# Optimization experiments

Measured on AMD Instinct MI355X. Metric: run time of the kernel, lower is better.

## Reference

```python
import jax, jax.numpy as jnp
import numpy as np

HEADS = 8
DIM_HEAD = 64
NB_FEATURES = 256
DIM = 512

def setup_inputs() -> dict:
    key = jax.random.key(0)
    ks = jax.random.split(key, 4)
    b, n = 2, 8192
    x = jax.random.normal(ks[0], (b, n, DIM), jnp.float32)
    # fan-in scaling so exp(feature projections) stays numerically sane
    Wqkv = jax.random.normal(ks[1], (3 * HEADS * DIM_HEAD, DIM), jnp.float32) / np.sqrt(DIM).astype(np.float32)
    Wout = jax.random.normal(ks[2], (DIM, HEADS * DIM_HEAD), jnp.float32) / np.sqrt(HEADS * DIM_HEAD).astype(np.float32)
    bout = jnp.zeros((DIM,), jnp.float32)
    proj = jax.random.normal(ks[3], (NB_FEATURES, DIM_HEAD), jnp.float32) / np.sqrt(DIM_HEAD).astype(np.float32)
    return {"x": x, "Wqkv": Wqkv, "Wout": Wout, "bout": bout, "proj": proj}

def reference(x, Wqkv, Wout, bout, proj):
    b, n, _ = x.shape
    scale = DIM_HEAD ** -0.5
    qkv = jnp.einsum('bnd,ed->bne', x, Wqkv)            # [b,n,3*h*dh]
    q, k, v = jnp.split(qkv, 3, axis=-1)
    to_heads = lambda t: t.reshape(b, n, HEADS, DIM_HEAD).transpose(0, 2, 1, 3)  # [b,h,n,dh]
    q = to_heads(q) * scale
    k = to_heads(k)
    v = to_heads(v)
    # FAVOR+ exp feature maps
    q_prime = jnp.exp(jnp.einsum('bhnd,fd->bhnf', q, proj))  # [b,h,n,f]
    k_prime = jnp.exp(jnp.einsum('bhnd,fd->bhnf', k, proj))  # [b,h,n,f]
    k_sum = k_prime.sum(axis=2)                              # [b,h,f]
    D = jnp.einsum('bhnf,bhf->bhn', q_prime, k_sum)          # normalizer
    D_inv = 1.0 / (D + 1e-6)
    context = jnp.einsum('bhmf,bhmd->bhfd', k_prime, v)      # [b,h,f,dh]
    out = jnp.einsum('bhnf,bhfd->bhnd', q_prime, context) * D_inv[..., None]
    out = out.transpose(0, 2, 1, 3).reshape(b, n, HEADS * DIM_HEAD)
    return jnp.einsum('bne,de->bnd', out, Wout) + bout
```

## Files before the change

kernel.cpp:

```cpp
#include <hip/hip_runtime.h>
#include <math.h>

#define B_    2
#define NSEQ  8192
#define DIM_  512
#define H_    8
#define DH_   64
#define F_    256
#define M_    (B_*NSEQ)
#define QKV_  1536

typedef __attribute__((ext_vector_type(8))) short     short8;
typedef __attribute__((ext_vector_type(4))) float     float4v;
typedef __attribute__((ext_vector_type(8))) unsigned short ushort8v;

__device__ __forceinline__ unsigned short f2bf(float f) {
    unsigned u = __float_as_uint(f);
    u += 0x7FFFu + ((u >> 16) & 1u);
    return (unsigned short)(u >> 16);
}
__device__ __forceinline__ float bf2f(unsigned short h) {
    unsigned u = ((unsigned)h) << 16;
    return __uint_as_float(u);
}
__device__ __forceinline__ unsigned pack2bf(float lo, float hi) {
    return __builtin_amdgcn_perm(__float_as_uint(hi), __float_as_uint(lo), 0x07060302);
}
__device__ __forceinline__ void glds16(const void* g, void* s) {
    __builtin_amdgcn_global_load_lds(
        (const __attribute__((address_space(1))) unsigned int*)g,
        (__attribute__((address_space(3))) unsigned int*)s, 16, 0, 0);
}

__global__ __launch_bounds__(256) void cvt_all(const float* __restrict__ x,
                                               const float* __restrict__ wqkv,
                                               const float* __restrict__ wout,
                                               const float* __restrict__ proj,
                                               unsigned short* __restrict__ xb,
                                               unsigned short* __restrict__ wqkvb,
                                               unsigned short* __restrict__ woutb,
                                               unsigned short* __restrict__ projb) {
    int bid = blockIdx.x;
    const float* in; unsigned short* out; int i;
    if (bid < 4096)      { in = x;    out = xb;    i = bid * 256 + threadIdx.x; }
    else if (bid < 4480) { in = wqkv; out = wqkvb; i = (bid - 4096) * 256 + threadIdx.x; }
    else if (bid < 4608) { in = wout; out = woutb; i = (bid - 4480) * 256 + threadIdx.x; }
    else                 { in = proj; out = projb; i = (bid - 4608) * 256 + threadIdx.x; }
    float4 a = ((const float4*)in)[2 * i];
    float4 b = ((const float4*)in)[2 * i + 1];
    ushort8v o;
    o[0] = f2bf(a.x); o[1] = f2bf(a.y); o[2] = f2bf(a.z); o[3] = f2bf(a.w);
    o[4] = f2bf(b.x); o[5] = f2bf(b.y); o[6] = f2bf(b.z); o[7] = f2bf(b.w);
    ((ushort8v*)out)[i] = o;
}

template<bool BF16OUT>
__global__ __launch_bounds__(512) void gemm_nt_pp(const unsigned short* __restrict__ A,
                                                  const unsigned short* __restrict__ Bm,
                                                  const float* __restrict__ bias,
                                                  void* __restrict__ Cout,
                                                  unsigned short* __restrict__ vTout,
                                                  int M, int N, int K) {
    __shared__ __align__(16) unsigned short As[3][32 * 512];
    __shared__ __align__(16) unsigned short Bs[3][16 * 512];
    const int t  = threadIdx.x;
    const int w  = t >> 6, l = t & 63;
    const int wm = w >> 1, wn = w & 1;
    const int lr = l & 15, lq = l >> 4;

    const int gx = gridDim.x;
    int flat = blockIdx.y * gx + blockIdx.x;
    int per  = (gx * gridDim.y) >> 3;
    int flat2 = (flat & 7) * per + (flat >> 3);
    const int m0 = (flat2 / gx) * 256, n0 = (flat2 % gx) * 128;

    float4v acc[4][4];
#pragma unroll
    for (int mi = 0; mi < 4; mi++)
#pragma unroll
        for (int ni = 0; ni < 4; ni++) acc[mi][ni] = (float4v){0.f, 0.f, 0.f, 0.f};

    auto stage = [&](int buf, int k0) {
#pragma unroll
        for (int i = 0; i < 4; i++) {
            int c = w * 4 + i, rb = c >> 1, ks = c & 1;
            glds16(A + (size_t)(m0 + rb * 16 + lr) * K + k0 + ks * 32 + lq * 8,
                   &As[buf][c * 512]);
        }
#pragma unroll
        for (int i = 0; i < 2; i++) {
            int c = w * 2 + i, rb = c >> 1, ks = c & 1;
            glds16(Bm + (size_t)(n0 + rb * 16 + lr) * K + k0 + ks * 32 + lq * 8,
                   &Bs[buf][c * 512]);
        }
    };

    stage(0, 0);
    stage(1, 64);

#pragma unroll
    for (int k = 0; k < 8; k++) {
        if (k < 7) { asm volatile("s_waitcnt vmcnt(6)" ::: "memory"); }
        else       { asm volatile("s_waitcnt vmcnt(0)" ::: "memory"); }
        __builtin_amdgcn_s_barrier();
        const int cur = k % 3;

        if (k + 2 < 8) stage((k + 2) % 3, (k + 2) << 6);

        short8 af[2][4], bfr[2][4];
#pragma unroll
        for (int ks = 0; ks < 2; ks++) {
#pragma unroll
            for (int mi = 0; mi < 4; mi++)
                af[ks][mi] = *(const short8*)&As[cur][(((wm * 4 + mi) * 2 + ks) * 64 + l) * 8];
#pragma unroll
            for (int ni = 0; ni < 4; ni++)
                bfr[ks][ni] = *(const short8*)&Bs[cur][(((wn * 4 + ni) * 2 + ks) * 64 + l) * 8];
        }

        __builtin_amdgcn_s_setprio(1);
#pragma unroll
        for (int ks = 0; ks < 2; ks++)
#pragma unroll
            for (int mi = 0; mi < 4; mi++)
#pragma unroll
                for (int ni = 0; ni < 4; ni++)
                    acc[mi][ni] = __builtin_amdgcn_mfma_f32_16x16x32_bf16(
                        af[ks][mi], bfr[ks][ni], acc[mi][ni], 0, 0, 0);
        __builtin_amdgcn_s_setprio(0);
    }

    const int q = l >> 4, c = l & 15;
#pragma unroll
    for (int mi = 0; mi < 4; mi++) {
        int row0 = m0 + wm * 64 + mi * 16 + q * 4;
#pragma unroll
        for (int ni = 0; ni < 4; ni++) {
            int col = n0 + wn * 64 + ni * 16 + c;
            if (BF16OUT && vTout != nullptr && col >= 1024) {
                int cm = col - 1024;
                int h2 = cm >> 6, dh = cm & 63;
                int bq = row0 >> 13;
                size_t nn = (size_t)(row0 & 8191);
                unsigned short* dst = vTout + (((size_t)bq * 8 + h2) * 64 + dh) * NSEQ + nn;
                uint2 pv;
                pv.x = ((unsigned)f2bf(acc[mi][ni][1]) << 16) | f2bf(acc[mi][ni][0]);
                pv.y = ((unsigned)f2bf(acc[mi][ni][3]) << 16) | f2bf(acc[mi][ni][2]);
                *(uint2*)dst = pv;
            } else {
                float bv = bias ? bias[col] : 0.f;
#pragma unroll
                for (int r = 0; r < 4; r++) {
                    float v = acc[mi][ni][r] + bv;
                    if (BF16OUT) ((unsigned short*)Cout)[(size_t)(row0 + r) * N + col] = f2bf(v);
                    else         ((float*)Cout)[(size_t)(row0 + r) * N + col] = v;
                }
            }
        }
    }
}

__global__ __launch_bounds__(256) void ctx_fused_mfma(
    const unsigned short* __restrict__ qkvb,
    const unsigned short* __restrict__ projb,
    const unsigned short* __restrict__ vT,
    unsigned short* __restrict__ partial)
{
    __shared__ __align__(16) unsigned short PB[16 * 512];
    __shared__ __align__(16) unsigned short KB[8 * 512];
    __shared__ __align__(16) unsigned short VB[8 * 512];
    __shared__ __align__(16) unsigned short KPA[16 * 512];
    const int t = threadIdx.x, w = t >> 6, l = t & 63;
    const int lr = l & 15, lq = l >> 4;
    const int s = blockIdx.x, fh = blockIdx.y, z = blockIdx.z;
    const int b = z >> 3, h = z & 7;
    const int nchunk = s * 512;

    for (int idx = w; idx < 16; idx += 4) {
        int fblk = idx >> 1, kt = idx & 1;
        glds16(projb + (size_t)(fh * 128 + fblk * 16 + lr) * 64 + kt * 32 + lq * 8, &PB[idx * 512]);
    }

    float4v acc[2][5];
#pragma unroll
    for (int mi = 0; mi < 2; mi++)
#pragma unroll
        for (int ni = 0; ni < 5; ni++) acc[mi][ni] = (float4v){0.f, 0.f, 0.f, 0.f};
    short ov = (lr == 0) ? (short)0x3F80 : (short)0;
    short8 ones = {ov, ov, ov, ov, ov, ov, ov, ov};

    for (int st = 0; st < 8; st++) {
        int nbase = nchunk + st * 64;
        __syncthreads();
        for (int idx = w; idx < 8; idx += 4) {
            int nblk = idx >> 1, kt = idx & 1;
            glds16(qkvb + ((size_t)b * NSEQ + nbase + nblk * 16 + lr) * QKV_ + 512 + h * 64 + kt * 32 + lq * 8,
                   &KB[idx * 512]);
        }
        for (int idx = w; idx < 8; idx += 4) {
            int dhb = idx >> 1, nt2 = idx & 1;
            glds16(vT + ((size_t)z * 64 + dhb * 16 + lr) * NSEQ + nbase + nt2 * 32 + lq * 8,
                   &VB[idx * 512]);
        }
        __syncthreads();

        float4v a2[4][2];
#pragma unroll
        for (int mi = 0; mi < 4; mi++)
#pragma unroll
            for (int ni = 0; ni < 2; ni++) a2[mi][ni] = (float4v){0.f, 0.f, 0.f, 0.f};
#pragma unroll
        for (int ks = 0; ks < 2; ks++) {
            short8 ka[4], pb[2];
#pragma unroll
            for (int mi = 0; mi < 4; mi++)
                ka[mi] = *(const short8*)&KB[((mi * 2 + ks) * 64 + l) * 8];
#pragma unroll
            for (int ni = 0; ni < 2; ni++)
                pb[ni] = *(const short8*)&PB[(((w * 2 + ni) * 2 + ks) * 64 + l) * 8];
#pragma unroll
            for (int mi = 0; mi < 4; mi++)
#pragma unroll
                for (int ni = 0; ni < 2; ni++)
                    a2[mi][ni] = __builtin_amdgcn_mfma_f32_16x16x32_bf16(ka[mi], pb[ni], a2[mi][ni], 0, 0, 0);
        }
#pragma unroll
        for (int mi = 0; mi < 4; mi++) {
            int nb = mi * 16 + lq * 4;
            int qoff = ((nb >> 3) & 3) * 256 + (nb & 7) * 2;
            int setn = nb >> 5;
#pragma unroll
            for (int ni = 0; ni < 2; ni++) {
                int fp = w * 32 + ni * 16 + lr;
                float e0 = __expf(a2[mi][ni][0]);
                float e1 = __expf(a2[mi][ni][1]);
                float e2 = __expf(a2[mi][ni][2]);
                float e3 = __expf(a2[mi][ni][3]);
                uint2 p; p.x = pack2bf(e0, e1); p.y = pack2bf(e2, e3);
                *(uint2*)((char*)KPA + (size_t)(((fp >> 4) * 2 + setn) * 1024 + qoff + (fp & 15) * 16)) = p;
            }
        }
#pragma unroll
        for (int ks = 0; ks < 2; ks++) {
            short8 af[2], bf[4];
#pragma unroll
            for (int mi = 0; mi < 2; mi++)
                af[mi] = *(const short8*)&KPA[(((w * 2 + mi) * 2 + ks) * 64 + l) * 8];
#pragma unroll
            for (int ni = 0; ni < 4; ni++)
                bf[ni] = *(const short8*)&VB[((ni * 2 + ks) * 64 + l) * 8];
#pragma unroll
            for (int mi = 0; mi < 2; mi++) {
#pragma unroll
                for (int ni = 0; ni < 4; ni++)
                    acc[mi][ni] = __builtin_amdgcn_mfma_f32_16x16x32_bf16(af[mi], bf[ni], acc[mi][ni], 0, 0, 0);
                acc[mi][4] = __builtin_amdgcn_mfma_f32_16x16x32_bf16(af[mi], ones, acc[mi][4], 0, 0, 0);
            }
        }
    }
    unsigned short* base = partial + (size_t)(s * 16 + z) * 80 * 256 + fh * 128;
#pragma unroll
    for (int mi = 0; mi < 2; mi++) {
        int f0r = w * 32 + mi * 16 + lq * 4;
#pragma unroll
        for (int ni = 0; ni < 5; ni++) {
            int col = ni * 16 + lr;
#pragma unroll
            for (int r = 0; r < 4; r++)
                base[(size_t)col * 256 + f0r + r] = f2bf(acc[mi][ni][r]);
        }
    }
}

__global__ __launch_bounds__(256) void ctx_reduce(const unsigned short* __restrict__ partial,
                                                  unsigned short* __restrict__ ctxT) {
    int idx8 = blockIdx.x * 256 + threadIdx.x;
    const int INNER = 16 * 80 * 256;
    size_t off = (size_t)idx8 * 8;
    float s0 = 0.f, s1 = 0.f, s2 = 0.f, s3 = 0.f, s4 = 0.f, s5 = 0.f, s6 = 0.f, s7 = 0.f;
#pragma unroll
    for (int k = 0; k < 16; k++) {
        ushort8v v = *(const ushort8v*)(partial + (size_t)k * INNER + off);
        s0 += bf2f(v[0]); s1 += bf2f(v[1]); s2 += bf2f(v[2]); s3 += bf2f(v[3]);
        s4 += bf2f(v[4]); s5 += bf2f(v[5]); s6 += bf2f(v[6]); s7 += bf2f(v[7]);
    }
    ushort8v o;
    o[0] = f2bf(s0); o[1] = f2bf(s1); o[2] = f2bf(s2); o[3] = f2bf(s3);
    o[4] = f2bf(s4); o[5] = f2bf(s5); o[6] = f2bf(s6); o[7] = f2bf(s7);
    *(ushort8v*)(ctxT + off) = o;
}

__global__ __launch_bounds__(256) void attn_fused_mfma(
    const unsigned short* __restrict__ qkvb,
    const unsigned short* __restrict__ projb,
    const unsigned short* __restrict__ ctxT,
    unsigned short* __restrict__ attnb)
{
    __shared__ __align__(16) unsigned short QB[16 * 512];
    __shared__ __align__(16) unsigned short PA[8 * 512];
    __shared__ __align__(16) unsigned short QPA[16 * 512];
    __shared__ __align__(16) unsigned short CB[10 * 512];
    const int t = threadIdx.x, w = t >> 6, l = t & 63;
    const int lr = l & 15, lq = l >> 4;
    const int m0 = blockIdx.x * 128, z = blockIdx.y;
    const int b = z >> 3, h = z & 7;

    for (int idx = w; idx < 16; idx += 4) {
        int mblk = idx >> 1, kt = idx & 1;
        glds16(qkvb + ((size_t)b * NSEQ + m0 + mblk * 16 + lr) * QKV_ + h * 64 + kt * 32 + lq * 8,
               &QB[idx * 512]);
    }
    float4v acc[2][5];
#pragma unroll
    for (int mi = 0; mi < 2; mi++)
#pragma unroll
        for (int ni = 0; ni < 5; ni++) acc[mi][ni] = (float4v){0.f, 0.f, 0.f, 0.f};

    for (int fs = 0; fs < 4; fs++) {
        int f0 = fs * 64;
        __syncthreads();
        for (int idx = w; idx < 8; idx += 4) {
            int fb = idx >> 1, kt = idx & 1;
            glds16(projb + (size_t)(f0 + fb * 16 + lr) * 64 + kt * 32 + lq * 8, &PA[idx * 512]);
        }
        for (int idx = w; idx < 10; idx += 4) {
            int dhb = idx >> 1, ft = idx & 1;
            glds16(ctxT + ((size_t)z * 80 + dhb * 16 + lr) * 256 + f0 + ft * 32 + lq * 8,
                   &CB[idx * 512]);
        }
        __syncthreads();

        float4v a2[4][2];
#pragma unroll
        for (int mi = 0; mi < 4; mi++)
#pragma unroll
            for (int ni = 0; ni < 2; ni++) a2[mi][ni] = (float4v){0.f, 0.f, 0.f, 0.f};
#pragma unroll
        for (int ks = 0; ks < 2; ks++) {
            short8 pa[4], qb[2];
#pragma unroll
            for (int mi = 0; mi < 4; mi++)
                pa[mi] = *(const short8*)&PA[((mi * 2 + ks) * 64 + l) * 8];
#pragma unroll
            for (int ni = 0; ni < 2; ni++)
                qb[ni] = *(const short8*)&QB[(((w * 2 + ni) * 2 + ks) * 64 + l) * 8];
#pragma unroll
            for (int mi = 0; mi < 4; mi++)
#pragma unroll
                for (int ni = 0; ni < 2; ni++)
                    a2[mi][ni] = __builtin_amdgcn_mfma_f32_16x16x32_bf16(pa[mi], qb[ni], a2[mi][ni], 0, 0, 0);
        }
#pragma unroll
        for (int mi = 0; mi < 4; mi++) {
            int fb2 = mi * 16 + lq * 4;
            int qoff = ((fb2 >> 3) & 3) * 256 + (fb2 & 7) * 2;
            int setf = fb2 >> 5;
#pragma unroll
            for (int ni = 0; ni < 2; ni++) {
                int m = w * 32 + ni * 16 + lr;
                float e0 = __expf(0.125f * a2[mi][ni][0]);
                float e1 = __expf(0.125f * a2[mi][ni][1]);
                float e2 = __expf(0.125f * a2[mi][ni][2]);
                float e3 = __expf(0.125f * a2[mi][ni][3]);
                uint2 p; p.x = pack2bf(e0, e1); p.y = pack2bf(e2, e3);
                *(uint2*)((char*)QPA + (size_t)(((m >> 4) * 2 + setf) * 1024 + qoff + (m & 15) * 16)) = p;
            }
        }
#pragma unroll
        for (int ks = 0; ks < 2; ks++) {
            short8 af[2], cb[5];
#pragma unroll
            for (int mi = 0; mi < 2; mi++)
                af[mi] = *(const short8*)&QPA[(((w * 2 + mi) * 2 + ks) * 64 + l) * 8];
#pragma unroll
            for (int ni = 0; ni < 5; ni++)
                cb[ni] = *(const short8*)&CB[((ni * 2 + ks) * 64 + l) * 8];
#pragma unroll
            for (int mi = 0; mi < 2; mi++)
#pragma unroll
                for (int ni = 0; ni < 5; ni++)
                    acc[mi][ni] = __builtin_amdgcn_mfma_f32_16x16x32_bf16(af[mi], cb[ni], acc[mi][ni], 0, 0, 0);
        }
    }
#pragma unroll
    for (int mi = 0; mi < 2; mi++) {
        int rowb = m0 + w * 32 + mi * 16 + lq * 4;
#pragma unroll
        for (int r = 0; r < 4; r++) {
            float dv = __shfl(acc[mi][4][r], (l & 48), 64);
            float rinv = 1.f / (dv + 1e-6f);
#pragma unroll
            for (int ni = 0; ni < 4; ni++)
                attnb[((size_t)b * NSEQ + rowb + r) * 512 + h * 64 + ni * 16 + lr] =
                    f2bf(acc[mi][ni][r] * rinv);
        }
    }
}

extern "C" void kernel_launch(void* const* d_in, const int* in_sizes, int n_in,
                              void* d_out, int out_size, void* d_ws, size_t ws_size,
                              hipStream_t stream) {
    const float* x    = (const float*)d_in[0];
    const float* Wqkv = (const float*)d_in[1];
    const float* Wout = (const float*)d_in[2];
    const float* bout = (const float*)d_in[3];
    const float* proj = (const float*)d_in[4];

    unsigned short* qkvb    = (unsigned short*)d_ws;
    unsigned short* vT      = qkvb + (size_t)M_ * QKV_;
    unsigned short* partial = vT + (size_t)16 * 64 * NSEQ;
    unsigned short* ctxT    = partial + (size_t)16 * 16 * 80 * 256;
    unsigned short* projb   = ctxT + (size_t)16 * 80 * 256;
    unsigned short* xb      = projb + 16384;
    unsigned short* attnb   = xb;
    unsigned short* wqkvb   = xb + (size_t)M_ * DIM_;
    unsigned short* woutb   = wqkvb + (size_t)QKV_ * DIM_;
    float* outp = (float*)d_out;

    cvt_all<<<dim3(4616), 256, 0, stream>>>(x, Wqkv, Wout, proj, xb, wqkvb, woutb, projb);
    gemm_nt_pp<true><<<dim3(QKV_ / 128, M_ / 256), 512, 0, stream>>>(xb, wqkvb, nullptr, qkvb, vT, M_, QKV_, DIM_);
    ctx_fused_mfma<<<dim3(16, 2, 16), 256, 0, stream>>>(qkvb, projb, vT, partial);
    ctx_reduce<<<dim3(160), 256, 0, stream>>>(partial, ctxT);
    attn_fused_mfma<<<dim3(64, 16), 256, 0, stream>>>(qkvb, projb, ctxT, attnb);
    gemm_nt_pp<false><<<dim3(DIM_ / 128, M_ / 256), 512, 0, stream>>>(attnb, woutb, bout, outp, nullptr, M_, DIM_, DIM_);
}
```

Before: 208.4 us.

## Split GEMM k-step into two half-phases interleaving LDS reads, prefetch and MFMA

Restructures the QKV GEMM main loop so each k-step runs as two halves. Each half reads part of the B fragments from LDS and issues half of the next-stage global-to-LDS loads, then runs the matching MFMAs, with extra barriers and sched_barriers to fix the ordering. The goal is to spread memory issue across the MFMA work and overlap loads with compute instead of bunching all staging at the start. It adds barriers per iteration, and the vmcnt accounting must stay correct for the triple-buffered pipeline.

```diff
diff --git a/kernel.cpp b/kernel.cpp
--- a/kernel.cpp
+++ b/kernel.cpp
@@ -80,54 +80,85 @@
 #pragma unroll
         for (int ni = 0; ni < 4; ni++) acc[mi][ni] = (float4v){0.f, 0.f, 0.f, 0.f};
 
-    auto stage = [&](int buf, int k0) {
-#pragma unroll
-        for (int i = 0; i < 4; i++) {
-            int c = w * 4 + i, rb = c >> 1, ks = c & 1;
-            glds16(A + (size_t)(m0 + rb * 16 + lr) * K + k0 + ks * 32 + lq * 8,
-                   &As[buf][c * 512]);
-        }
-#pragma unroll
-        for (int i = 0; i < 2; i++) {
-            int c = w * 2 + i, rb = c >> 1, ks = c & 1;
-            glds16(Bm + (size_t)(n0 + rb * 16 + lr) * K + k0 + ks * 32 + lq * 8,
-                   &Bs[buf][c * 512]);
-        }
+    auto stageA = [&](int buf, int k0, int i) {
+        int c = w * 4 + i, rb = c >> 1, ks = c & 1;
+        glds16(A + (size_t)(m0 + rb * 16 + lr) * K + k0 + ks * 32 + lq * 8,
+               &As[buf][c * 512]);
     };
-
-    stage(0, 0);
-    stage(1, 64);
+    auto stageB = [&](int buf, int k0, int i) {
+        int c = w * 2 + i, rb = c >> 1, ks = c & 1;
+        glds16(Bm + (size_t)(n0 + rb * 16 + lr) * K + k0 + ks * 32 + lq * 8,
+               &Bs[buf][c * 512]);
+    };
+
+#pragma unroll
+    for (int i = 0; i < 4; i++) stageA(0, 0, i);
+#pragma unroll
+    for (int i = 0; i < 2; i++) stageB(0, 0, i);
+#pragma unroll
+    for (int i = 0; i < 4; i++) stageA(1, 64, i);
+#pragma unroll
+    for (int i = 0; i < 2; i++) stageB(1, 64, i);
+    asm volatile("s_waitcnt vmcnt(6)" ::: "memory");
+    __builtin_amdgcn_s_barrier();
 
 #pragma unroll
     for (int k = 0; k < 8; k++) {
-        if (k < 7) { asm volatile("s_waitcnt vmcnt(6)" ::: "memory"); }
-        else       { asm volatile("s_waitcnt vmcnt(0)" ::: "memory"); }
+        const int cur = k % 3;
+        const int nxt = (k + 2) % 3;
+        const int kn  = (k + 2) << 6;
+        const bool pf = (k < 6);
+
+        short8 a[2][4], b[2][4];
+
+#pragma unroll
+        for (int ks = 0; ks < 2; ks++)
+#pragma unroll
+            for (int mi = 0; mi < 4; mi++)
+                a[ks][mi] = *(const short8*)&As[cur][(((wm * 4 + mi) * 2 + ks) * 64 + l) * 8];
+#pragma unroll
+        for (int ks = 0; ks < 2; ks++)
+#pragma unroll
+            for (int ni = 0; ni < 2; ni++)
+                b[ks][ni] = *(const short8*)&Bs[cur][(((wn * 4 + ni) * 2 + ks) * 64 + l) * 8];
+        if (pf) { stageA(nxt, kn, 0); stageA(nxt, kn, 1); stageB(nxt, kn, 0); }
         __builtin_amdgcn_s_barrier();
-        const int cur = k % 3;
-
-        if (k + 2 < 8) stage((k + 2) % 3, (k + 2) << 6);
-
-        short8 af[2][4], bfr[2][4];
-#pragma unroll
-        for (int ks = 0; ks < 2; ks++) {
-#pragma unroll
-            for (int mi = 0; mi < 4; mi++)
-                af[ks][mi] = *(const short8*)&As[cur][(((wm * 4 + mi) * 2 + ks) * 64 + l) * 8];
-#pragma unroll
-            for (int ni = 0; ni < 4; ni++)
-                bfr[ks][ni] = *(const short8*)&Bs[cur][(((wn * 4 + ni) * 2 + ks) * 64 + l) * 8];
-        }
-
+        asm volatile("s_waitcnt lgkmcnt(0)" ::: "memory");
+        __builtin_amdgcn_sched_barrier(0);
         __builtin_amdgcn_s_setprio(1);
 #pragma unroll
         for (int ks = 0; ks < 2; ks++)
 #pragma unroll
             for (int mi = 0; mi < 4; mi++)
 #pragma unroll
-                for (int ni = 0; ni < 4; ni++)
+                for (int ni = 0; ni < 2; ni++)
                     acc[mi][ni] = __builtin_amdgcn_mfma_f32_16x16x32_bf16(
-                        af[ks][mi], bfr[ks][ni], acc[mi][ni], 0, 0, 0);
+                        a[ks][mi], b[ks][ni], acc[mi][ni], 0, 0, 0);
         __builtin_amdgcn_s_setprio(0);
+        __builtin_amdgcn_s_barrier();
+
+#pragma unroll
+        for (int ks = 0; ks < 2; ks++)
+#pragma unroll
+            for (int ni = 2; ni < 4; ni++)
+                b[ks][ni] = *(const short8*)&Bs[cur][(((wn * 4 + ni) * 2 + ks) * 64 + l) * 8];
+        if (pf) { stageA(nxt, kn, 2); stageA(nxt, kn, 3); stageB(nxt, kn, 1); }
+        __builtin_amdgcn_s_barrier();
+        asm volatile("s_waitcnt lgkmcnt(0)" ::: "memory");
+        __builtin_amdgcn_sched_barrier(0);
+        __builtin_amdgcn_s_setprio(1);
+#pragma unroll
+        for (int ks = 0; ks < 2; ks++)
+#pragma unroll
+            for (int mi = 0; mi < 4; mi++)
+#pragma unroll
+                for (int ni = 2; ni < 4; ni++)
+                    acc[mi][ni] = __builtin_amdgcn_mfma_f32_16x16x32_bf16(
+                        a[ks][mi], b[ks][ni], acc[mi][ni], 0, 0, 0);
+        __builtin_amdgcn_s_setprio(0);
+        if (k < 6)       { asm volatile("s_waitcnt vmcnt(6)" ::: "memory"); }
+        else if (k == 6) { asm volatile("s_waitcnt vmcnt(0)" ::: "memory"); }
+        __builtin_amdgcn_s_barrier();
     }
 
     const int q = l >> 4, c = l & 15;
```

Result: no change. 209.7 us (+0.6%).

## Shrink QKV GEMM tile to 128x128 with K32 stages; widen ctx_reduce grid

Applied to the files above, without the earlier changes.

The QKV projection GEMM now uses 128x128 tiles, 256 threads and 32-wide K stages in a runtime K loop, which quadruples the block count to raise occupancy and wave count. The old 256x128 kernel is kept as a dedicated output-projection GEMM. ctx_reduce now handles two elements per thread with four times as many blocks, for more parallelism on a small reduction. The trade-off is less data reuse per tile, more barriers per K step, and narrower memory accesses in the reduce.

```diff
diff --git a/kernel.cpp b/kernel.cpp
--- a/kernel.cpp
+++ b/kernel.cpp
@@ -55,14 +55,14 @@
 }
 
 template<bool BF16OUT>
-__global__ __launch_bounds__(512) void gemm_nt_pp(const unsigned short* __restrict__ A,
+__global__ __launch_bounds__(256) void gemm_nt_pp(const unsigned short* __restrict__ A,
                                                   const unsigned short* __restrict__ Bm,
                                                   const float* __restrict__ bias,
                                                   void* __restrict__ Cout,
                                                   unsigned short* __restrict__ vTout,
                                                   int M, int N, int K) {
-    __shared__ __align__(16) unsigned short As[3][32 * 512];
-    __shared__ __align__(16) unsigned short Bs[3][16 * 512];
+    __shared__ __align__(16) unsigned short As[3][128 * 32];
+    __shared__ __align__(16) unsigned short Bs[3][128 * 32];
     const int t  = threadIdx.x;
     const int w  = t >> 6, l = t & 63;
     const int wm = w >> 1, wn = w & 1;
@@ -72,7 +72,7 @@
     int flat = blockIdx.y * gx + blockIdx.x;
     int per  = (gx * gridDim.y) >> 3;
     int flat2 = (flat & 7) * per + (flat >> 3);
-    const int m0 = (flat2 / gx) * 256, n0 = (flat2 % gx) * 128;
+    const int m0 = (flat2 / gx) * 128, n0 = (flat2 % gx) * 128;
 
     float4v acc[4][4];
 #pragma unroll
@@ -82,51 +82,41 @@
 
     auto stage = [&](int buf, int k0) {
 #pragma unroll
-        for (int i = 0; i < 4; i++) {
-            int c = w * 4 + i, rb = c >> 1, ks = c & 1;
-            glds16(A + (size_t)(m0 + rb * 16 + lr) * K + k0 + ks * 32 + lq * 8,
-                   &As[buf][c * 512]);
-        }
-#pragma unroll
         for (int i = 0; i < 2; i++) {
-            int c = w * 2 + i, rb = c >> 1, ks = c & 1;
-            glds16(Bm + (size_t)(n0 + rb * 16 + lr) * K + k0 + ks * 32 + lq * 8,
-                   &Bs[buf][c * 512]);
+            int rb8 = w * 2 + i;
+            int row = rb8 * 16 + lr;
+            glds16(A + (size_t)(m0 + row) * K + k0 + lq * 8, &As[buf][rb8 * 512]);
+            glds16(Bm + (size_t)(n0 + row) * K + k0 + lq * 8, &Bs[buf][rb8 * 512]);
         }
     };
 
+    const int nk = K >> 5;
     stage(0, 0);
-    stage(1, 64);
-
-#pragma unroll
-    for (int k = 0; k < 8; k++) {
-        if (k < 7) { asm volatile("s_waitcnt vmcnt(6)" ::: "memory"); }
-        else       { asm volatile("s_waitcnt vmcnt(0)" ::: "memory"); }
+    stage(1, 32);
+
+    for (int k = 0; k < nk; k++) {
+        if (k + 1 < nk) { asm volatile("s_waitcnt vmcnt(4)" ::: "memory"); }
+        else            { asm volatile("s_waitcnt vmcnt(0)" ::: "memory"); }
         __builtin_amdgcn_s_barrier();
+
         const int cur = k % 3;
-
-        if (k + 2 < 8) stage((k + 2) % 3, (k + 2) << 6);
-
-        short8 af[2][4], bfr[2][4];
-#pragma unroll
-        for (int ks = 0; ks < 2; ks++) {
-#pragma unroll
-            for (int mi = 0; mi < 4; mi++)
-                af[ks][mi] = *(const short8*)&As[cur][(((wm * 4 + mi) * 2 + ks) * 64 + l) * 8];
+        if (k + 2 < nk) stage((k + 2) % 3, (k + 2) << 5);
+
+        short8 af[4], bfr[4];
+#pragma unroll
+        for (int mi = 0; mi < 4; mi++)
+            af[mi] = *(const short8*)&As[cur][((wm * 4 + mi) * 64 + l) * 8];
+#pragma unroll
+        for (int ni = 0; ni < 4; ni++)
+            bfr[ni] = *(const short8*)&Bs[cur][((wn * 4 + ni) * 64 + l) * 8];
+
+        __builtin_amdgcn_s_setprio(1);
+#pragma unroll
+        for (int mi = 0; mi < 4; mi++)
 #pragma unroll
             for (int ni = 0; ni < 4; ni++)
-                bfr[ks][ni] = *(const short8*)&Bs[cur][(((wn * 4 + ni) * 2 + ks) * 64 + l) * 8];
-        }
-
-        __builtin_amdgcn_s_setprio(1);
-#pragma unroll
-        for (int ks = 0; ks < 2; ks++)
-#pragma unroll
-            for (int mi = 0; mi < 4; mi++)
-#pragma unroll
-                for (int ni = 0; ni < 4; ni++)
-                    acc[mi][ni] = __builtin_amdgcn_mfma_f32_16x16x32_bf16(
-                        af[ks][mi], bfr[ks][ni], acc[mi][ni], 0, 0, 0);
+                acc[mi][ni] = __builtin_amdgcn_mfma_f32_16x16x32_bf16(
+                    af[mi], bfr[ni], acc[mi][ni], 0, 0, 0);
         __builtin_amdgcn_s_setprio(0);
     }
 
@@ -156,6 +146,95 @@
                     else         ((float*)Cout)[(size_t)(row0 + r) * N + col] = v;
                 }
             }
+        }
+    }
+}
+
+__global__ __launch_bounds__(512) void gemm_out_256(const unsigned short* __restrict__ A,
+                                                    const unsigned short* __restrict__ Bm,
+                                                    const float* __restrict__ bias,
+                                                    float* __restrict__ Cout,
+                                                    int M, int N, int K) {
+    __shared__ __align__(16) unsigned short As[3][32 * 512];
+    __shared__ __align__(16) unsigned short Bs[3][16 * 512];
+    const int t  = threadIdx.x;
+    const int w  = t >> 6, l = t & 63;
+    const int wm = w >> 1, wn = w & 1;
+    const int lr = l & 15, lq = l >> 4;
+
+    const int gx = gridDim.x;
+    int flat = blockIdx.y * gx + blockIdx.x;
+    int per  = (gx * gridDim.y) >> 3;
+    int flat2 = (flat & 7) * per + (flat >> 3);
+    const int m0 = (flat2 / gx) * 256, n0 = (flat2 % gx) * 128;
+
+    float4v acc[4][4];
+#pragma unroll
+    for (int mi = 0; mi < 4; mi++)
+#pragma unroll
+        for (int ni = 0; ni < 4; ni++) acc[mi][ni] = (float4v){0.f, 0.f, 0.f, 0.f};
+
+    auto stage = [&](int buf, int k0) {
+#pragma unroll
+        for (int i = 0; i < 4; i++) {
+            int c = w * 4 + i, rb = c >> 1, ks = c & 1;
+            glds16(A + (size_t)(m0 + rb * 16 + lr) * K + k0 + ks * 32 + lq * 8,
+                   &As[buf][c * 512]);
+        }
+#pragma unroll
+        for (int i = 0; i < 2; i++) {
+            int c = w * 2 + i, rb = c >> 1, ks = c & 1;
+            glds16(Bm + (size_t)(n0 + rb * 16 + lr) * K + k0 + ks * 32 + lq * 8,
+                   &Bs[buf][c * 512]);
+        }
+    };
+
+    stage(0, 0);
+    stage(1, 64);
+
+#pragma unroll
+    for (int k = 0; k < 8; k++) {
+        if (k < 7) { asm volatile("s_waitcnt vmcnt(6)" ::: "memory"); }
+        else       { asm volatile("s_waitcnt vmcnt(0)" ::: "memory"); }
+        __builtin_amdgcn_s_barrier();
+        const int cur = k % 3;
+
+        if (k + 2 < 8) stage((k + 2) % 3, (k + 2) << 6);
+
+        short8 af[2][4], bfr[2][4];
+#pragma unroll
+        for (int ks = 0; ks < 2; ks++) {
+#pragma unroll
+            for (int mi = 0; mi < 4; mi++)
+                af[ks][mi] = *(const short8*)&As[cur][(((wm * 4 + mi) * 2 + ks) * 64 + l) * 8];
+#pragma unroll
+            for (int ni = 0; ni < 4; ni++)
+                bfr[ks][ni] = *(const short8*)&Bs[cur][(((wn * 4 + ni) * 2 + ks) * 64 + l) * 8];
+        }
+
+        __builtin_amdgcn_s_setprio(1);
+#pragma unroll
+        for (int ks = 0; ks < 2; ks++)
+#pragma unroll
+            for (int mi = 0; mi < 4; mi++)
+#pragma unroll
+                for (int ni = 0; ni < 4; ni++)
+                    acc[mi][ni] = __builtin_amdgcn_mfma_f32_16x16x32_bf16(
+                        af[ks][mi], bfr[ks][ni], acc[mi][ni], 0, 0, 0);
+        __builtin_amdgcn_s_setprio(0);
+    }
+
+    const int q = l >> 4, c = l & 15;
+#pragma unroll
+    for (int mi = 0; mi < 4; mi++) {
+        int row0 = m0 + wm * 64 + mi * 16 + q * 4;
+#pragma unroll
+        for (int ni = 0; ni < 4; ni++) {
+            int col = n0 + wn * 64 + ni * 16 + c;
+            float bv = bias ? bias[col] : 0.f;
+#pragma unroll
+            for (int r = 0; r < 4; r++)
+                Cout[(size_t)(row0 + r) * N + col] = acc[mi][ni][r] + bv;
         }
     }
 }
@@ -274,20 +353,17 @@
 
 __global__ __launch_bounds__(256) void ctx_reduce(const unsigned short* __restrict__ partial,
                                                   unsigned short* __restrict__ ctxT) {
-    int idx8 = blockIdx.x * 256 + threadIdx.x;
+    int idx2 = blockIdx.x * 256 + threadIdx.x;
     const int INNER = 16 * 80 * 256;
-    size_t off = (size_t)idx8 * 8;
-    float s0 = 0.f, s1 = 0.f, s2 = 0.f, s3 = 0.f, s4 = 0.f, s5 = 0.f, s6 = 0.f, s7 = 0.f;
+    size_t off = (size_t)idx2 * 2;
+    float s0 = 0.f, s1 = 0.f;
 #pragma unroll
     for (int k = 0; k < 16; k++) {
-        ushort8v v = *(const ushort8v*)(partial + (size_t)k * INNER + off);
-        s0 += bf2f(v[0]); s1 += bf2f(v[1]); s2 += bf2f(v[2]); s3 += bf2f(v[3]);
-        s4 += bf2f(v[4]); s5 += bf2f(v[5]); s6 += bf2f(v[6]); s7 += bf2f(v[7]);
-    }
-    ushort8v o;
-    o[0] = f2bf(s0); o[1] = f2bf(s1); o[2] = f2bf(s2); o[3] = f2bf(s3);
-    o[4] = f2bf(s4); o[5] = f2bf(s5); o[6] = f2bf(s6); o[7] = f2bf(s7);
-    *(ushort8v*)(ctxT + off) = o;
+        unsigned v = *(const unsigned*)(partial + (size_t)k * INNER + off);
+        s0 += bf2f((unsigned short)(v & 0xffffu));
+        s1 += bf2f((unsigned short)(v >> 16));
+    }
+    *(unsigned*)(ctxT + off) = ((unsigned)f2bf(s1) << 16) | f2bf(s0);
 }
 
 __global__ __launch_bounds__(256) void attn_fused_mfma(
@@ -418,9 +494,9 @@
     float* outp = (float*)d_out;
 
     cvt_all<<<dim3(4616), 256, 0, stream>>>(x, Wqkv, Wout, proj, xb, wqkvb, woutb, projb);
-    gemm_nt_pp<true><<<dim3(QKV_ / 128, M_ / 256), 512, 0, stream>>>(xb, wqkvb, nullptr, qkvb, vT, M_, QKV_, DIM_);
+    gemm_nt_pp<true><<<dim3(QKV_ / 128, M_ / 128), 256, 0, stream>>>(xb, wqkvb, nullptr, qkvb, vT, M_, QKV_, DIM_);
     ctx_fused_mfma<<<dim3(16, 2, 16), 256, 0, stream>>>(qkvb, projb, vT, partial);
-    ctx_reduce<<<dim3(160), 256, 0, stream>>>(partial, ctxT);
+    ctx_reduce<<<dim3(640), 256, 0, stream>>>(partial, ctxT);
     attn_fused_mfma<<<dim3(64, 16), 256, 0, stream>>>(qkvb, projb, ctxT, attnb);
-    gemm_nt_pp<false><<<dim3(DIM_ / 128, M_ / 256), 512, 0, stream>>>(attnb, woutb, bout, outp, nullptr, M_, DIM_, DIM_);
-}
+    gemm_out_256<<<dim3(DIM_ / 128, M_ / 256), 512, 0, stream>>>(attnb, woutb, bout, outp, M_, DIM_, DIM_);
+}
```

Result: no change. 211.4 us (+1.4%).
